# Performance work log

Measured on AMD Instinct MI355X. Metric: run time of the kernel, lower is better.

## Reference

```python
import jax, jax.numpy as jnp
import numpy as np

HEADS = 12
D_MODEL = 768
D_K = D_MODEL // HEADS
BS, SEQ = 2, 4096


def setup_inputs() -> dict:
    key = jax.random.key(0)
    ks = jax.random.split(key, 12)
    s = 1.0 / np.sqrt(D_MODEL)
    return {
        "q": jax.random.normal(ks[0], (BS, SEQ, D_MODEL), jnp.float32),
        "k": jax.random.normal(ks[1], (BS, SEQ, D_MODEL), jnp.float32),
        "v": jax.random.normal(ks[2], (BS, SEQ, D_MODEL), jnp.float32),
        "Wq": jax.random.normal(ks[3], (D_MODEL, D_MODEL), jnp.float32) * s,
        "bq": jax.random.normal(ks[4], (D_MODEL,), jnp.float32) * s,
        "Wk": jax.random.normal(ks[5], (D_MODEL, D_MODEL), jnp.float32) * s,
        "bk": jax.random.normal(ks[6], (D_MODEL,), jnp.float32) * s,
        "Wv": jax.random.normal(ks[7], (D_MODEL, D_MODEL), jnp.float32) * s,
        "bv": jax.random.normal(ks[8], (D_MODEL,), jnp.float32) * s,
        "Wo": jax.random.normal(ks[9], (D_MODEL, D_MODEL), jnp.float32) * s,
        "bo": jax.random.normal(ks[10], (D_MODEL,), jnp.float32) * s,
        "mask": jnp.ones((BS, 1, SEQ), jnp.int32),
    }


def reference(q, k, v, Wq, bq, Wk, bk, Wv, bv, Wo, bo, mask):
    bs, sq, _ = q.shape
    # torch Linear: x @ W.T + b; then reshape to (bs, S, h, d_k) and transpose to (bs, h, S, d_k)
    def proj(x, W, b):
        y = x @ W.T + b
        return y.reshape(bs, -1, HEADS, D_K).transpose(0, 2, 1, 3)
    qh, kh, vh = proj(q, Wq, bq), proj(k, Wk, bk), proj(v, Wv, bv)
    scores = jnp.einsum("bhqd,bhkd->bhqk", qh, kh) / np.sqrt(D_K)
    # mask.unsqueeze(1): [bs,1,1,S_kv], masked_fill where mask == 0
    scores = jnp.where(mask[:, None, :, :] == 0, jnp.float32(-1e9), scores)
    attn = jax.nn.softmax(scores, axis=-1)  # dropout = identity (eval mode)
    ctx = jnp.einsum("bhqk,bhkd->bhqd", attn, vh)
    concat = ctx.transpose(0, 2, 1, 3).reshape(bs, sq, D_MODEL)
    return concat @ Wo.T + bo
```

## Files before the change

kernel.cpp:

```cpp
#include <hip/hip_runtime.h>
#include <hip/hip_bf16.h>

typedef __bf16 bf16x8 __attribute__((ext_vector_type(8)));
typedef __bf16 bf16x4 __attribute__((ext_vector_type(4)));
typedef float f32x4 __attribute__((ext_vector_type(4)));
typedef unsigned short u16;

#define HEADS 12
#define DK 64
#define DM 768
#define SEQL 4096
#define BSZ 2
#define MROWS (BSZ * SEQL)
#define WELEM (DM * DM)
#define NX 6291456
#define WTOT (4 * WELEM)
#define BTOT (4 * 768)

#define QSCALE 0.180336880434245f
#define EXP2F(x) __builtin_amdgcn_exp2f(x)

__device__ __forceinline__ float bf2f(u16 x) {
    unsigned int u = ((unsigned int)x) << 16;
    return __uint_as_float(u);
}
__device__ __forceinline__ u16 f2bf(float f) {
    unsigned int u = __float_as_uint(f);
    u += 0x7fff + ((u >> 16) & 1);
    return (u16)(u >> 16);
}
__device__ __forceinline__ unsigned int cvt_pk(float lo, float hi) {
#if __has_builtin(__builtin_amdgcn_cvt_pk_bf16_f32)
    auto r = __builtin_amdgcn_cvt_pk_bf16_f32(lo, hi);
    unsigned int u;
    __builtin_memcpy(&u, &r, 4);
    return u;
#else
    return (unsigned int)f2bf(lo) | ((unsigned int)f2bf(hi) << 16);
#endif
}

__global__ void detect_dtype(const u16* __restrict__ q, int* __restrict__ flag) {
    __shared__ int cnt;
    if (threadIdx.x == 0) cnt = 0;
    __syncthreads();
    int c = 0;
    for (int i = threadIdx.x; i < 16384; i += 256) {
        u16 x = q[i];
        if (((x >> 7) & 0xFF) == 0xFF) c++;
    }
    if (c) atomicAdd(&cnt, c);
    __syncthreads();
    if (threadIdx.x == 0) *flag = (cnt > 0) ? 1 : 0;
}

__global__ __launch_bounds__(256) void convert_x(
    const void* __restrict__ X0, const void* __restrict__ X1, const void* __restrict__ X2,
    u16* __restrict__ Xc, const int* __restrict__ flag) {
    const int f32m = *flag;
    int i8 = blockIdx.x * 256 + threadIdx.x;
    if (i8 >= 3 * NX / 8) return;
    int w = i8 / (NX / 8);
    int off8 = i8 - w * (NX / 8);
    const void* src = (w == 0) ? X0 : (w == 1) ? X1 : X2;
    u16* dst = Xc + (size_t)w * NX + (size_t)off8 * 8;
    if (f32m) {
        float4 f0 = ((const float4*)src)[off8 * 2];
        float4 f1 = ((const float4*)src)[off8 * 2 + 1];
        uint4 p = {cvt_pk(f0.x, f0.y), cvt_pk(f0.z, f0.w),
                   cvt_pk(f1.x, f1.y), cvt_pk(f1.z, f1.w)};
        *(uint4*)dst = p;
    } else {
        *(uint4*)dst = ((const uint4*)src)[off8];
    }
}

__global__ __launch_bounds__(256) void convert_wb(
    const void* __restrict__ W0, const void* __restrict__ W1,
    const void* __restrict__ W2, const void* __restrict__ W3,
    const void* __restrict__ B0, const void* __restrict__ B1,
    const void* __restrict__ B2, const void* __restrict__ B3,
    u16* __restrict__ Wc, u16* __restrict__ bc, const int* __restrict__ flag) {
    const int f32m = *flag;
    int i4 = blockIdx.x * 256 + threadIdx.x;
    const int n4 = (WTOT + BTOT) / 4;
    if (i4 >= n4) return;
    int base = i4 * 4;
    const void* src;
    u16* dst;
    int off;
    if (base < WTOT) {
        int w = base / WELEM;
        off = base - w * WELEM;
        src = (w == 0) ? W0 : (w == 1) ? W1 : (w == 2) ? W2 : W3;
        dst = Wc + w * WELEM + off;
    } else {
        int bi = base - WTOT;
        int w = bi / 768;
        off = bi - w * 768;
        src = (w == 0) ? B0 : (w == 1) ? B1 : (w == 2) ? B2 : B3;
        dst = bc + w * 768 + off;
    }
    if (f32m) {
        float4 f = *(const float4*)((const float*)src + off);
        uint2 p = {cvt_pk(f.x, f.y), cvt_pk(f.z, f.w)};
        *(uint2*)dst = p;
    } else {
        *(uint2*)dst = *(const uint2*)((const u16*)src + off);
    }
}

typedef __attribute__((address_space(1))) unsigned int glb_u32;
typedef __attribute__((address_space(3))) unsigned int lds_u32;

__device__ __forceinline__ void gld16(const u16* g, u16* l) {
    __builtin_amdgcn_global_load_lds((glb_u32*)g, (lds_u32*)l, 16, 0, 0);
}

template <int NCH>
__device__ __forceinline__ void stage_g(const u16* gbase, u16* lbase, int tid) {
#pragma unroll
    for (int it = 0; it < NCH / 256; ++it) {
        int c = it * 256 + tid;
        int row = c >> 2, p = c & 3;
        int gc = p ^ (row & 3);
        gld16(gbase + (size_t)row * DM + gc * 8, lbase + c * 8);
    }
}

__global__ __launch_bounds__(256) void gemm_qkv3(
    const u16* __restrict__ X0, const u16* __restrict__ X1, const u16* __restrict__ X2,
    const u16* __restrict__ Wc, const u16* __restrict__ bc,
    u16* __restrict__ Yq, u16* __restrict__ Yk, u16* __restrict__ Yv) {
    __shared__ __align__(16) u16 SM[2][2][128 * 32];

    const int by  = blockIdx.y;
    const int sel = by / 6;
    const int n0  = (by - sel * 6) * 128;
    const int m0  = blockIdx.x * 128;

    const u16* X  = sel == 0 ? X0 : (sel == 1 ? X1 : X2);
    const u16* W  = Wc + (size_t)sel * WELEM;
    const u16* Bp = bc + sel * 768;
    u16* Y = sel == 0 ? Yq : (sel == 1 ? Yk : Yv);
    const float oscale = sel == 0 ? QSCALE : 1.0f;

    const int tid = threadIdx.x, lane = tid & 63, wave = tid >> 6;
    const int wr = (wave >> 1) * 64, wc2 = (wave & 1) * 64;
    const int l15 = lane & 15, quad = lane >> 4;
    const int ck = (quad ^ (l15 & 3)) * 8;

    f32x4 acc[4][4] = {};

    stage_g<512>(X + (size_t)m0 * DM, &SM[0][0][0], tid);
    stage_g<512>(W + (size_t)n0 * DM, &SM[1][0][0], tid);
    __syncthreads();

    for (int it = 0; it < 24; ++it) {
        const int cur = it & 1, nxt = cur ^ 1;
        if (it < 23) {
            stage_g<512>(X + (size_t)m0 * DM + (it + 1) * 32, &SM[0][nxt][0], tid);
            stage_g<512>(W + (size_t)n0 * DM + (it + 1) * 32, &SM[1][nxt][0], tid);
        }
        bf16x8 a[4], b[4];
#pragma unroll
        for (int i = 0; i < 4; ++i)
            a[i] = *(const bf16x8*)&SM[0][cur][(wr + i * 16 + l15) * 32 + ck];
#pragma unroll
        for (int j = 0; j < 4; ++j)
            b[j] = *(const bf16x8*)&SM[1][cur][(wc2 + j * 16 + l15) * 32 + ck];
        if (sel < 2) {
#pragma unroll
            for (int i = 0; i < 4; ++i)
#pragma unroll
                for (int j = 0; j < 4; ++j)
                    acc[i][j] = __builtin_amdgcn_mfma_f32_16x16x32_bf16(b[j], a[i], acc[i][j], 0, 0, 0);
        } else {
#pragma unroll
            for (int i = 0; i < 4; ++i)
#pragma unroll
                for (int j = 0; j < 4; ++j)
                    acc[i][j] = __builtin_amdgcn_mfma_f32_16x16x32_bf16(a[i], b[j], acc[i][j], 0, 0, 0);
        }
        __syncthreads();
    }

    u16* eb = &SM[0][0][0] + wave * 4096;
    const int r7l = l15 & 7;
    const int hh = (n0 + wc2) >> 6;

    if (sel < 2) {
        f32x4 bj[4];
#pragma unroll
        for (int j = 0; j < 4; ++j) {
            uint2 bb4 = *(const uint2*)&Bp[n0 + wc2 + j * 16 + quad * 4];
            bj[j][0] = bf2f((u16)(bb4.x & 0xffff));
            bj[j][1] = bf2f((u16)(bb4.x >> 16));
            bj[j][2] = bf2f((u16)(bb4.y & 0xffff));
            bj[j][3] = bf2f((u16)(bb4.y >> 16));
        }
#pragma unroll
        for (int i = 0; i < 4; ++i) {
            int Yl = i * 16 + l15;
#pragma unroll
            for (int j = 0; j < 4; ++j) {
                float v0 = (acc[i][j][0] + bj[j][0]) * oscale;
                float v1 = (acc[i][j][1] + bj[j][1]) * oscale;
                float v2 = (acc[i][j][2] + bj[j][2]) * oscale;
                float v3 = (acc[i][j][3] + bj[j][3]) * oscale;
                uint2 cv = {cvt_pk(v0, v1), cvt_pk(v2, v3)};
                int ch = (j * 4 + quad) ^ (r7l * 2);
                *(uint2*)&eb[Yl * 64 + ch * 4] = cv;
            }
        }
        asm volatile("" ::: "memory");
#pragma unroll
        for (int it2 = 0; it2 < 8; ++it2) {
            int Yp = it2 * 8 + (lane >> 3);
            int sc = ((lane & 7) * 2) ^ ((Yp & 7) * 2);
            uint4 w = *(const uint4*)&eb[Yp * 64 + sc * 4];
            int row0 = m0 + wr + Yp;
            int bb = row0 >> 12, s0 = row0 & (SEQL - 1);
            *(uint4*)&Y[(((size_t)(bb * HEADS + hh)) << 18) + (s0 << 6) + (lane & 7) * 8] = w;
        }
    } else {
#pragma unroll
        for (int j = 0; j < 4; ++j) {
            int Yl = j * 16 + l15;
            float bv = bf2f(Bp[n0 + wc2 + Yl]);
#pragma unroll
            for (int i = 0; i < 4; ++i) {
                uint2 cv = {cvt_pk(acc[i][j][0] + bv, acc[i][j][1] + bv),
                            cvt_pk(acc[i][j][2] + bv, acc[i][j][3] + bv)};
                int ch = (i * 4 + quad) ^ (r7l * 2);
                *(uint2*)&eb[Yl * 64 + ch * 4] = cv;
            }
        }
        asm volatile("" ::: "memory");
        const int bb = (m0 + wr) >> 12, s0 = (m0 + wr) & (SEQL - 1);
#pragma unroll
        for (int it2 = 0; it2 < 8; ++it2) {
            int Yp = it2 * 8 + (lane >> 3);
            int sc = ((lane & 7) * 2) ^ ((Yp & 7) * 2);
            uint4 w = *(const uint4*)&eb[Yp * 64 + sc * 4];
            *(uint4*)&Y[(((size_t)(bb * HEADS + hh)) << 18) + ((size_t)Yp << 12) + s0 + (lane & 7) * 8] = w;
        }
    }
}

__global__ __launch_bounds__(256) void gemm_out3(const u16* __restrict__ X,
                                                 const u16* __restrict__ W,
                                                 const u16* __restrict__ Bp,
                                                 void* __restrict__ Y,
                                                 const int* __restrict__ flag) {
    __shared__ __align__(16) u16 As[2][64 * 32];
    __shared__ __align__(16) u16 Bs[2][128 * 32];

    const int f32mode = *flag;
    const int m0 = blockIdx.x * 64, n0 = blockIdx.y * 128;
    const int tid = threadIdx.x, lane = tid & 63, wave = tid >> 6;
    const int wr = (wave >> 1) * 32, wc2 = (wave & 1) * 64;
    const int l15 = lane & 15, quad = lane >> 4;
    const int ck = (quad ^ (l15 & 3)) * 8;

    f32x4 acc[2][4] = {};

    stage_g<256>(X + (size_t)m0 * DM, &As[0][0], tid);
    stage_g<512>(W + (size_t)n0 * DM, &Bs[0][0], tid);
    __syncthreads();

    for (int it = 0; it < 24; ++it) {
        const int cur = it & 1, nxt = cur ^ 1;
        if (it < 23) {
            stage_g<256>(X + (size_t)m0 * DM + (it + 1) * 32, &As[nxt][0], tid);
            stage_g<512>(W + (size_t)n0 * DM + (it + 1) * 32, &Bs[nxt][0], tid);
        }
        bf16x8 a[2], b[4];
#pragma unroll
        for (int i = 0; i < 2; ++i)
            a[i] = *(const bf16x8*)&As[cur][(wr + i * 16 + l15) * 32 + ck];
#pragma unroll
        for (int j = 0; j < 4; ++j)
            b[j] = *(const bf16x8*)&Bs[cur][(wc2 + j * 16 + l15) * 32 + ck];
#pragma unroll
        for (int i = 0; i < 2; ++i)
#pragma unroll
            for (int j = 0; j < 4; ++j)
                acc[i][j] = __builtin_amdgcn_mfma_f32_16x16x32_bf16(a[i], b[j], acc[i][j], 0, 0, 0);
        __syncthreads();
    }

#pragma unroll
    for (int j = 0; j < 4; ++j) {
        int o = n0 + wc2 + j * 16 + l15;
        float bv = bf2f(Bp[o]);
#pragma unroll
        for (int i = 0; i < 2; ++i)
#pragma unroll
            for (int r = 0; r < 4; ++r) {
                int row = m0 + wr + i * 16 + quad * 4 + r;
                float val = acc[i][j][r] + bv;
                if (f32mode) ((float*)Y)[(size_t)row * DM + o] = val;
                else         ((u16*)Y)[(size_t)row * DM + o] = f2bf(val);
            }
    }
}

__device__ __forceinline__ void stage8_bf16(u16* dst, const u16* src) {
    *(uint4*)dst = *(const uint4*)src;
}
__device__ __forceinline__ void stage16_bf16(u16* dst, const u16* src) {
    *(uint4*)dst = *(const uint4*)src;
    *(uint4*)(dst + 8) = *(const uint4*)(src + 8);
}
__device__ __forceinline__ void stage16_f32pk(u16* dst, const float* src) {
    float4 f0 = ((const float4*)src)[0];
    float4 f1 = ((const float4*)src)[1];
    float4 f2 = ((const float4*)src)[2];
    float4 f3 = ((const float4*)src)[3];
    uint4 lo = {cvt_pk(f0.x, f0.y), cvt_pk(f0.z, f0.w), cvt_pk(f1.x, f1.y), cvt_pk(f1.z, f1.w)};
    uint4 hi = {cvt_pk(f2.x, f2.y), cvt_pk(f2.z, f2.w), cvt_pk(f3.x, f3.y), cvt_pk(f3.z, f3.w)};
    *(uint4*)dst = lo;
    *(uint4*)(dst + 8) = hi;
}

__global__ __launch_bounds__(256) void gemm_qkv_fb(
    const void* __restrict__ Xq, const void* __restrict__ Xk, const void* __restrict__ Xv,
    const u16* __restrict__ Wc, const u16* __restrict__ bc,
    u16* __restrict__ Yq, u16* __restrict__ Yk, u16* __restrict__ Yv,
    const int* __restrict__ flag) {
    __shared__ __align__(16) u16 As[128][40];
    __shared__ __align__(16) u16 Bs[64][40];
    const int f32mode = *flag;
    const int by = blockIdx.y;
    const int sel = by / 12;
    const int n0 = (by - sel * 12) * 64;
    const int m0 = blockIdx.x * 128;
    const void* Xp = sel == 0 ? Xq : (sel == 1 ? Xk : Xv);
    const u16* Wp = Wc + sel * WELEM;
    const u16* Bp = bc + sel * 768;
    u16* Y = sel == 0 ? Yq : (sel == 1 ? Yk : Yv);
    const float oscale = sel == 0 ? QSCALE : 1.0f;
    const int tid = threadIdx.x, lane = tid & 63, wave = tid >> 6;
    const int wr = (wave >> 1) * 64, wc = (wave & 1) * 32;
    const int l15 = lane & 15, quad = lane >> 4;
    const int srA = tid >> 1, scA = (tid & 1) * 16;
    const int srB = tid >> 2, scB = (tid & 3) * 8;
    f32x4 acc[4][2] = {};
    const size_t xoff = (size_t)(m0 + srA) * DM + scA;
    const size_t woff = (size_t)(n0 + srB) * DM + scB;
    for (int kb = 0; kb < DM; kb += 32) {
        if (f32mode) stage16_f32pk(&As[srA][scA], (const float*)Xp + xoff + kb);
        else         stage16_bf16(&As[srA][scA], (const u16*)Xp + xoff + kb);
        stage8_bf16(&Bs[srB][scB], Wp + woff + kb);
        __syncthreads();
        bf16x8 a[4], b[2];
#pragma unroll
        for (int i = 0; i < 4; ++i) a[i] = *(const bf16x8*)&As[wr + i * 16 + l15][quad * 8];
#pragma unroll
        for (int j = 0; j < 2; ++j) b[j] = *(const bf16x8*)&Bs[wc + j * 16 + l15][quad * 8];
#pragma unroll
        for (int i = 0; i < 4; ++i)
#pragma unroll
            for (int j = 0; j < 2; ++j)
                acc[i][j] = __builtin_amdgcn_mfma_f32_16x16x32_bf16(a[i], b[j], acc[i][j], 0, 0, 0);
        __syncthreads();
    }
#pragma unroll
    for (int j = 0; j < 2; ++j) {
        int o = n0 + wc + j * 16 + l15;
        float bv = bf2f(Bp[o]);
#pragma unroll
        for (int i = 0; i < 4; ++i)
#pragma unroll
            for (int r = 0; r < 4; ++r) {
                int row = m0 + wr + i * 16 + quad * 4 + r;
                float val = (acc[i][j][r] + bv) * oscale;
                int bb = row >> 12, s = row & (SEQL - 1);
                int h = o >> 6, d = o & 63;
                if (sel < 2) Y[((bb * HEADS + h) << 18) + (s << 6) + d] = f2bf(val);
                else         Y[((bb * HEADS + h) << 18) + (d << 12) + s] = f2bf(val);
            }
    }
}

__global__ __launch_bounds__(256) void gemm_out_fb(const u16* __restrict__ X,
                                                   const u16* __restrict__ Wp,
                                                   const u16* __restrict__ Bp,
                                                   void* __restrict__ Y,
                                                   const int* __restrict__ flag) {
    __shared__ __align__(16) u16 As[128][40];
    __shared__ __align__(16) u16 Bs[64][40];
    const int f32mode = *flag;
    const int m0 = blockIdx.x * 128, n0 = blockIdx.y * 64;
    const int tid = threadIdx.x, lane = tid & 63, wave = tid >> 6;
    const int wr = (wave >> 1) * 64, wc = (wave & 1) * 32;
    const int l15 = lane & 15, quad = lane >> 4;
    const int srA = tid >> 1, scA = (tid & 1) * 16;
    const int srB = tid >> 2, scB = (tid & 3) * 8;
    f32x4 acc[4][2] = {};
    const size_t xoff = (size_t)(m0 + srA) * DM + scA;
    const size_t woff = (size_t)(n0 + srB) * DM + scB;
    for (int kb = 0; kb < DM; kb += 32) {
        stage16_bf16(&As[srA][scA], X + xoff + kb);
        stage8_bf16(&Bs[srB][scB], Wp + woff + kb);
        __syncthreads();
        bf16x8 a[4], b[2];
#pragma unroll
        for (int i = 0; i < 4; ++i) a[i] = *(const bf16x8*)&As[wr + i * 16 + l15][quad * 8];
#pragma unroll
        for (int j = 0; j < 2; ++j) b[j] = *(const bf16x8*)&Bs[wc + j * 16 + l15][quad * 8];
#pragma unroll
        for (int i = 0; i < 4; ++i)
#pragma unroll
            for (int j = 0; j < 2; ++j)
                acc[i][j] = __builtin_amdgcn_mfma_f32_16x16x32_bf16(a[i], b[j], acc[i][j], 0, 0, 0);
        __syncthreads();
    }
#pragma unroll
    for (int j = 0; j < 2; ++j) {
        int o = n0 + wc + j * 16 + l15;
        float bv = bf2f(Bp[o]);
#pragma unroll
        for (int i = 0; i < 4; ++i)
#pragma unroll
            for (int r = 0; r < 4; ++r) {
                int row = m0 + wr + i * 16 + quad * 4 + r;
                float val = acc[i][j][r] + bv;
                if (f32mode) ((float*)Y)[(size_t)row * DM + o] = val;
                else         ((u16*)Y)[(size_t)row * DM + o] = f2bf(val);
            }
    }
}

__device__ __forceinline__ void stage_tile(const u16* gbase, int rstride,
                                           u16* lbase, int tid) {
#pragma unroll
    for (int it = 0; it < 2; ++it) {
        int c = it * 256 + tid;
        int row = c >> 3, p = c & 7;
        int gc = p ^ (row & 7);
        gld16(gbase + (size_t)row * rstride + gc * 8, lbase + c * 8);
    }
}

__global__ __launch_bounds__(256, 3) void flash_attn(const u16* __restrict__ Q,
                                                     const u16* __restrict__ K,
                                                     const u16* __restrict__ Vt,
                                                     const int* __restrict__ mask,
                                                     u16* __restrict__ ctx) {
    __shared__ __align__(16) u16 KVs[2][2][64 * 64];
    __shared__ __align__(16) float Ms[2][64];
    __shared__ int Mf[2];
    __shared__ int AnyM;

    const int tid  = threadIdx.x;
    const int lane = tid & 63;
    const int wave = tid >> 6;
    const int l15  = lane & 15;
    const int quad = lane >> 4;

    const int bh = blockIdx.y;
    const int b  = bh / HEADS;
    const int h  = bh - b * HEADS;
    const int qb = blockIdx.x * 128 + wave * 32;

    const u16* Qh = Q  + ((size_t)bh << 18);
    const u16* Kh = K  + ((size_t)bh << 18);
    const u16* Vh = Vt + ((size_t)bh << 18);
    const int* maskb = mask + b * SEQL;

    if (tid == 0) AnyM = 0;
    int zf = 0;
#pragma unroll
    for (int i = 0; i < 16; ++i) zf |= (maskb[tid + i * 256] == 0);

    bf16x8 aq[2][2];
#pragma unroll
    for (int s = 0; s < 2; ++s)
#pragma unroll
        for (int c = 0; c < 2; ++c)
            aq[s][c] = *(const bf16x8*)&Qh[(size_t)(qb + s * 16 + l15) * DK + c * 32 + quad * 8];

    __syncthreads();
    if (zf) atomicOr(&AnyM, 1);
    __syncthreads();
    const int anym = AnyM;

    const int r7   = l15 & 7;
    const int ck0  = (quad ^ r7) * 8;
    const int ck1  = ((quad + 4) ^ r7) * 8;
    const int lrow = l15 * 64;
    const int vq   = quad >> 1;
    const int voff = (quad & 1) * 4;

    float m_s[2] = {-3.0e38f, -3.0e38f};
    float l_s[2] = {0.f, 0.f};
    f32x4 o_acc[2][4] = {};

    stage_tile(Kh, DK, &KVs[0][0][0], tid);
    stage_tile(Vh, SEQL, &KVs[0][1][0], tid);
    int mreg = 0;
    if (anym && tid < 64) {
        mreg = maskb[tid];
        int anyt = __any(mreg == 0);
        Ms[0][tid] = (mreg == 0) ? -1.0e9f : 0.0f;
        if (tid == 0) Mf[0] = anyt;
        mreg = maskb[64 + tid];
    }
    __syncthreads();

#pragma unroll 2
    for (int t = 0; t < 64; ++t) {
        const int cur = t & 1, nxt = cur ^ 1;
        if (t < 63) {
            const int kt = (t + 1) * 64;
            stage_tile(Kh + (size_t)kt * DK, DK, &KVs[nxt][0][0], tid);
            stage_tile(Vh + kt, SEQL, &KVs[nxt][1][0], tid);
            if (anym && tid < 64) {
                int anyt = __any(mreg == 0);
                Ms[nxt][tid] = (mreg == 0) ? -1.0e9f : 0.0f;
                if (tid == 0) Mf[nxt] = anyt;
                if (t < 62) mreg = maskb[(t + 2) * 64 + tid];
            }
        }

        const u16* kb2 = &KVs[cur][0][0];
        const u16* vb  = &KVs[cur][1][0];

        f32x4 s4[2][4];
#pragma unroll
        for (int nt = 0; nt < 4; ++nt) {
            bf16x8 ak0 = *(const bf16x8*)&kb2[lrow + nt * 1024 + ck0];
            bf16x8 ak1 = *(const bf16x8*)&kb2[lrow + nt * 1024 + ck1];
#pragma unroll
            for (int s = 0; s < 2; ++s) {
                f32x4 z = {};
                z = __builtin_amdgcn_mfma_f32_16x16x32_bf16(ak0, aq[s][0], z, 0, 0, 0);
                z = __builtin_amdgcn_mfma_f32_16x16x32_bf16(ak1, aq[s][1], z, 0, 0, 0);
                s4[s][nt] = z;
            }
        }

        bf16x8 av[4][2];
#pragma unroll
        for (int dv = 0; dv < 4; ++dv) {
            const u16* vr = &vb[(dv * 16 + l15) * 64];
#pragma unroll
            for (int kbi = 0; kbi < 2; ++kbi) {
                uint2 lo = *(const uint2*)&vr[((kbi * 4 + vq) ^ r7) * 8 + voff];
                uint2 hi = *(const uint2*)&vr[((kbi * 4 + 2 + vq) ^ r7) * 8 + voff];
                uint4 cc = {lo.x, lo.y, hi.x, hi.y};
                __builtin_memcpy(&av[dv][kbi], &cc, 16);
            }
        }

        const int usebias = anym ? Mf[cur] : 0;
        if (usebias) {
#pragma unroll
            for (int nt = 0; nt < 4; ++nt) {
                f32x4 bias = *(const f32x4*)&Ms[cur][nt * 16 + quad * 4];
#pragma unroll
                for (int s = 0; s < 2; ++s)
#pragma unroll
                    for (int r = 0; r < 4; ++r) s4[s][nt][r] += bias[r];
            }
        }

        float mx2[2];
#pragma unroll
        for (int s = 0; s < 2; ++s) {
            float a0 = fmaxf(fmaxf(s4[s][0][0], s4[s][0][1]), s4[s][0][2]);
            float a1 = fmaxf(fmaxf(s4[s][0][3], s4[s][1][0]), s4[s][1][1]);
            float a2 = fmaxf(fmaxf(s4[s][1][2], s4[s][1][3]), s4[s][2][0]);
            float a3 = fmaxf(fmaxf(s4[s][2][1], s4[s][2][2]), s4[s][2][3]);
            float a4 = fmaxf(fmaxf(s4[s][3][0], s4[s][3][1]), s4[s][3][2]);
            float b0 = fmaxf(fmaxf(a0, a1), a2);
            float b1 = fmaxf(fmaxf(a3, a4), s4[s][3][3]);
            float mx = fmaxf(b0, b1);
            mx = fmaxf(mx, __shfl_xor(mx, 16, 64));
            mx = fmaxf(mx, __shfl_xor(mx, 32, 64));
            mx2[s] = mx;
        }

        if (!__all((mx2[0] <= m_s[0] + 8.f) && (mx2[1] <= m_s[1] + 8.f))) {
#pragma unroll
            for (int s = 0; s < 2; ++s) {
                float newm = fmaxf(m_s[s], mx2[s]);
                float alpha = EXP2F(m_s[s] - newm);
                l_s[s] *= alpha;
#pragma unroll
                for (int dv = 0; dv < 4; ++dv) o_acc[s][dv] *= alpha;
                m_s[s] = newm;
            }
        }

#pragma unroll
        for (int s = 0; s < 2; ++s) {
            f32x4 ps = {};
#pragma unroll
            for (int nt = 0; nt < 4; ++nt) {
                f32x4 e = s4[s][nt] - m_s[s];
                e[0] = EXP2F(e[0]); e[1] = EXP2F(e[1]);
                e[2] = EXP2F(e[2]); e[3] = EXP2F(e[3]);
                s4[s][nt] = e;
                ps += e;
            }
            l_s[s] += (ps[0] + ps[1]) + (ps[2] + ps[3]);
        }

        bf16x8 pp[2][2];
#pragma unroll
        for (int s = 0; s < 2; ++s)
#pragma unroll
            for (int kbi = 0; kbi < 2; ++kbi) {
                uint4 cv = {cvt_pk(s4[s][2 * kbi][0],     s4[s][2 * kbi][1]),
                            cvt_pk(s4[s][2 * kbi][2],     s4[s][2 * kbi][3]),
                            cvt_pk(s4[s][2 * kbi + 1][0], s4[s][2 * kbi + 1][1]),
                            cvt_pk(s4[s][2 * kbi + 1][2], s4[s][2 * kbi + 1][3])};
                __builtin_memcpy(&pp[s][kbi], &cv, 16);
            }

        __builtin_amdgcn_s_setprio(1);
#pragma unroll
        for (int kbi = 0; kbi < 2; ++kbi)
#pragma unroll
            for (int dv = 0; dv < 4; ++dv)
#pragma unroll
                for (int s = 0; s < 2; ++s)
                    o_acc[s][dv] = __builtin_amdgcn_mfma_f32_16x16x32_bf16(
                        av[dv][kbi], pp[s][kbi], o_acc[s][dv], 0, 0, 0);
        __builtin_amdgcn_s_setprio(0);
        __syncthreads();
    }

    u16* eb = &KVs[0][0][0] + wave * 2304;
#pragma unroll
    for (int s = 0; s < 2; ++s) {
        float lf = l_s[s];
        lf += __shfl_xor(lf, 16, 64);
        lf += __shfl_xor(lf, 32, 64);
        float inv = 1.0f / lf;
#pragma unroll
        for (int dv = 0; dv < 4; ++dv) {
            uint2 cv = {cvt_pk(o_acc[s][dv][0] * inv, o_acc[s][dv][1] * inv),
                        cvt_pk(o_acc[s][dv][2] * inv, o_acc[s][dv][3] * inv)};
            *(uint2*)&eb[(s * 16 + l15) * 72 + dv * 16 + quad * 4] = cv;
        }
    }
    asm volatile("" ::: "memory");
    {
        int rowq = lane >> 2, dchunk = lane & 3;
#pragma unroll
        for (int s = 0; s < 2; ++s) {
            uint4 w0 = *(const uint4*)&eb[(s * 16 + rowq) * 72 + dchunk * 16];
            uint4 w1 = *(const uint4*)&eb[(s * 16 + rowq) * 72 + dchunk * 16 + 8];
            size_t orow = (size_t)(b * SEQL + qb + s * 16 + rowq) * DM + h * DK + dchunk * 16;
            *(uint4*)&ctx[orow] = w0;
            *(uint4*)&ctx[orow + 8] = w1;
        }
    }
}

extern "C" void kernel_launch(void* const* d_in, const int* in_sizes, int n_in,
                              void* d_out, int out_size, void* d_ws, size_t ws_size,
                              hipStream_t stream) {
    const void* q   = d_in[0];
    const void* k   = d_in[1];
    const void* v   = d_in[2];
    const void* Wq  = d_in[3];
    const void* bq  = d_in[4];
    const void* Wk  = d_in[5];
    const void* bk  = d_in[6];
    const void* Wv  = d_in[7];
    const void* bv  = d_in[8];
    const void* Wo  = d_in[9];
    const void* bo  = d_in[10];
    const int* mask = (const int*)d_in[11];

    const size_t NSH = (size_t)NX;
    u16* ws = (u16*)d_ws;

    const size_t need_full = (6 * NSH + WTOT + BTOT) * sizeof(u16) + 64;
    const size_t need_fb   = (4 * NSH + WTOT + BTOT) * sizeof(u16) + 64;

    if (ws_size >= need_full) {
        u16* Qh  = ws;
        u16* Kh  = ws + NSH;
        u16* Vth = ws + 2 * NSH;
        u16* Xc  = ws + 3 * NSH;
        u16* ctx = Xc;
        u16* Wc  = ws + 6 * NSH;
        u16* bc  = Wc + WTOT;
        int* dflag = (int*)(bc + BTOT);

        detect_dtype<<<1, 256, 0, stream>>>((const u16*)q, dflag);
        convert_x<<<(3 * NX / 8 + 255) / 256, 256, 0, stream>>>(q, k, v, Xc, dflag);
        convert_wb<<<((WTOT + BTOT) / 4 + 255) / 256, 256, 0, stream>>>(
            Wq, Wk, Wv, Wo, bq, bk, bv, bo, Wc, bc, dflag);

        gemm_qkv3<<<dim3(MROWS / 128, 18), 256, 0, stream>>>(
            Xc, Xc + NSH, Xc + 2 * NSH, Wc, bc, Qh, Kh, Vth);
        flash_attn<<<dim3(SEQL / 128, BSZ * HEADS), 256, 0, stream>>>(Qh, Kh, Vth, mask, ctx);
        gemm_out3<<<dim3(MROWS / 64, 6), 256, 0, stream>>>(
            ctx, Wc + 3 * (size_t)WELEM, bc + 3 * 768, d_out, dflag);
    } else if (ws_size >= need_fb) {
        u16* Qh  = ws;
        u16* Kh  = ws + NSH;
        u16* Vth = ws + 2 * NSH;
        u16* ctx = ws + 3 * NSH;
        u16* Wc  = ws + 4 * NSH;
        u16* bc  = Wc + WTOT;
        int* dflag = (int*)(bc + BTOT);

        detect_dtype<<<1, 256, 0, stream>>>((const u16*)q, dflag);
        convert_wb<<<((WTOT + BTOT) / 4 + 255) / 256, 256, 0, stream>>>(
            Wq, Wk, Wv, Wo, bq, bk, bv, bo, Wc, bc, dflag);
        gemm_qkv_fb<<<dim3(MROWS / 128, 36), 256, 0, stream>>>(
            q, k, v, Wc, bc, Qh, Kh, Vth, dflag);
        flash_attn<<<dim3(SEQL / 128, BSZ * HEADS), 256, 0, stream>>>(Qh, Kh, Vth, mask, ctx);
        gemm_out_fb<<<dim3(MROWS / 128, 12), 256, 0, stream>>>(
            ctx, Wc + 3 * (size_t)WELEM, bc + 3 * 768, d_out, dflag);
    }
}
```

Measured before the change: 402.2 us.

## Remap block indices for L2/XCD locality, drop lazy rescale, defer V loads

Remaps the linear block index in the QKV GEMM, output GEMM and flash attention kernels so that blocks landing on the same XCD share A/B tiles or the same batch-head. The aim is better L2 reuse across the MI355X chiplets. In flash attention it replaces the thresholded lazy max rescale with an exact check that rescales whenever the max changes, which may rescale more often. It also moves the V fragment LDS reads after softmax, shortening register live ranges and reducing pressure.

```diff
diff --git a/kernel.cpp b/kernel.cpp
--- a/kernel.cpp
+++ b/kernel.cpp
@@ -134,10 +134,14 @@
     u16* __restrict__ Yq, u16* __restrict__ Yk, u16* __restrict__ Yv) {
     __shared__ __align__(16) u16 SM[2][2][128 * 32];
 
-    const int by  = blockIdx.y;
-    const int sel = by / 6;
-    const int n0  = (by - sel * 6) * 128;
-    const int m0  = blockIdx.x * 128;
+    const int L   = blockIdx.y * 64 + blockIdx.x;
+    const int g   = L >> 3;
+    const int bxn = (L & 7) * 8 + (g & 7);
+    const int byn = g >> 3;
+
+    const int sel = byn / 6;
+    const int n0  = (byn - sel * 6) * 128;
+    const int m0  = bxn * 128;
 
     const u16* X  = sel == 0 ? X0 : (sel == 1 ? X1 : X2);
     const u16* W  = Wc + (size_t)sel * WELEM;
@@ -257,7 +261,10 @@
     __shared__ __align__(16) u16 Bs[2][128 * 32];
 
     const int f32mode = *flag;
-    const int m0 = blockIdx.x * 64, n0 = blockIdx.y * 128;
+    const int L  = blockIdx.y * 128 + blockIdx.x;
+    const int g  = L >> 3;
+    const int m0 = ((L & 7) * 16 + (g & 15)) * 64;
+    const int n0 = (g >> 4) * 128;
     const int tid = threadIdx.x, lane = tid & 63, wave = tid >> 6;
     const int wr = (wave >> 1) * 32, wc2 = (wave & 1) * 64;
     const int l15 = lane & 15, quad = lane >> 4;
@@ -460,10 +467,14 @@
     const int l15  = lane & 15;
     const int quad = lane >> 4;
 
-    const int bh = blockIdx.y;
+    const int L  = blockIdx.y * 32 + blockIdx.x;
+    const int gg = L >> 3;
+    const int bh = (L & 7) * 3 + (gg >> 5);
+    const int qblk = gg & 31;
+
     const int b  = bh / HEADS;
     const int h  = bh - b * HEADS;
-    const int qb = blockIdx.x * 128 + wave * 32;
+    const int qb = qblk * 128 + wave * 32;
 
     const u16* Qh = Q  + ((size_t)bh << 18);
     const u16* Kh = K  + ((size_t)bh << 18);
@@ -541,20 +552,6 @@
                 s4[s][nt] = z;
             }
         }
-
-        bf16x8 av[4][2];
-#pragma unroll
-        for (int dv = 0; dv < 4; ++dv) {
-            const u16* vr = &vb[(dv * 16 + l15) * 64];
-#pragma unroll
-            for (int kbi = 0; kbi < 2; ++kbi) {
-                uint2 lo = *(const uint2*)&vr[((kbi * 4 + vq) ^ r7) * 8 + voff];
-                uint2 hi = *(const uint2*)&vr[((kbi * 4 + 2 + vq) ^ r7) * 8 + voff];
-                uint4 cc = {lo.x, lo.y, hi.x, hi.y};
-                __builtin_memcpy(&av[dv][kbi], &cc, 16);
-            }
-        }
-
         const int usebias = anym ? Mf[cur] : 0;
         if (usebias) {
 #pragma unroll
@@ -567,7 +564,7 @@
             }
         }
 
-        float mx2[2];
+        float newm[2];
 #pragma unroll
         for (int s = 0; s < 2; ++s) {
             float a0 = fmaxf(fmaxf(s4[s][0][0], s4[s][0][1]), s4[s][0][2]);
@@ -580,18 +577,17 @@
             float mx = fmaxf(b0, b1);
             mx = fmaxf(mx, __shfl_xor(mx, 16, 64));
             mx = fmaxf(mx, __shfl_xor(mx, 32, 64));
-            mx2[s] = mx;
-        }
-
-        if (!__all((mx2[0] <= m_s[0] + 8.f) && (mx2[1] <= m_s[1] + 8.f))) {
+            newm[s] = fmaxf(m_s[s], mx);
+        }
+
+        if (!__all(newm[0] == m_s[0] && newm[1] == m_s[1])) {
 #pragma unroll
             for (int s = 0; s < 2; ++s) {
-                float newm = fmaxf(m_s[s], mx2[s]);
-                float alpha = EXP2F(m_s[s] - newm);
+                float alpha = EXP2F(m_s[s] - newm[s]);
                 l_s[s] *= alpha;
 #pragma unroll
                 for (int dv = 0; dv < 4; ++dv) o_acc[s][dv] *= alpha;
-                m_s[s] = newm;
+                m_s[s] = newm[s];
             }
         }
 
@@ -600,7 +596,7 @@
             f32x4 ps = {};
 #pragma unroll
             for (int nt = 0; nt < 4; ++nt) {
-                f32x4 e = s4[s][nt] - m_s[s];
+                f32x4 e = s4[s][nt] - newm[s];
                 e[0] = EXP2F(e[0]); e[1] = EXP2F(e[1]);
                 e[2] = EXP2F(e[2]); e[3] = EXP2F(e[3]);
                 s4[s][nt] = e;
@@ -620,6 +616,19 @@
                             cvt_pk(s4[s][2 * kbi + 1][2], s4[s][2 * kbi + 1][3])};
                 __builtin_memcpy(&pp[s][kbi], &cv, 16);
             }
+
+        bf16x8 av[4][2];
+#pragma unroll
+        for (int dv = 0; dv < 4; ++dv) {
+            const u16* vr = &vb[(dv * 16 + l15) * 64];
+#pragma unroll
+            for (int kbi = 0; kbi < 2; ++kbi) {
+                uint2 lo = *(const uint2*)&vr[((kbi * 4 + vq) ^ r7) * 8 + voff];
+                uint2 hi = *(const uint2*)&vr[((kbi * 4 + 2 + vq) ^ r7) * 8 + voff];
+                uint4 cc = {lo.x, lo.y, hi.x, hi.y};
+                __builtin_memcpy(&av[dv][kbi], &cc, 16);
+            }
+        }
 
         __builtin_amdgcn_s_setprio(1);
 #pragma unroll
```

Result: faster. 386.1 us (-4.0%).
